# Performance work log

Hardware: AMD Instinct MI355X
Metric: run time of the kernel (lower is better)

The kernel has to match this reference:

```python
import jax, jax.numpy as jnp
import numpy as np

B, S, D, H = 4, 2048, 1024, 16
HD = D // H


def setup_inputs() -> dict:
    key = jax.random.key(0)
    ks = jax.random.split(key, 9)
    s = 0.02  # GPT-2 init scale for weights
    return {
        "hidden_states": jax.random.normal(ks[0], (B, S, D), jnp.float32),
        "Wq": jax.random.normal(ks[1], (D, D), jnp.float32) * s,
        "bq": jnp.zeros((D,), jnp.float32),
        "Wk": jax.random.normal(ks[2], (D, D), jnp.float32) * s,
        "bk": jnp.zeros((D,), jnp.float32),
        "Wv": jax.random.normal(ks[3], (D, D), jnp.float32) * s,
        "bv": jnp.zeros((D,), jnp.float32),
        "Wo": jax.random.normal(ks[4], (D, D), jnp.float32) * s,
        "bo": jnp.zeros((D,), jnp.float32),
    }


def _split_heads(x):
    b, s, _ = x.shape
    return x.reshape(b, s, H, HD).transpose(0, 2, 1, 3)  # [B,H,S,HD]


def reference(hidden_states, Wq, bq, Wk, bk, Wv, bv, Wo, bo):
    b, s, d = hidden_states.shape
    q = _split_heads(hidden_states @ Wq + bq)
    k = _split_heads(hidden_states @ Wk + bk)
    v = _split_heads(hidden_states @ Wv + bv)
    # naive attention: full [B,H,S,S] scores, scale, causal where-mask, softmax, AV
    scores = jnp.einsum('bhqd,bhkd->bhqk', q, k)
    scores = scores / jnp.asarray(HD, scores.dtype) ** 0.5  # scale_attn_weights
    causal = jnp.tril(jnp.ones((s, s), dtype=bool))  # bias buffer slice
    scores = jnp.where(causal, scores, jnp.finfo(scores.dtype).min)
    attn = jax.nn.softmax(scores, axis=-1)  # attn_dropout p=0 -> identity
    out = jnp.einsum('bhqk,bhkd->bhqd', attn, v)
    out = out.transpose(0, 2, 1, 3).reshape(b, s, d)  # merge heads
    return out @ Wo + bo  # resid_dropout p=0 -> identity
```

## Files before the change

kernel.cpp:

```cpp
#include <hip/hip_runtime.h>
#include <stdint.h>


#define GAS __attribute__((address_space(1)))
#define LAS __attribute__((address_space(3)))

typedef __attribute__((ext_vector_type(4))) float f32x4;
typedef __attribute__((ext_vector_type(8))) short bf16x8;

__device__ __forceinline__ short f2bf(float f) {
  union { float f; uint32_t u; } v; v.f = f;
  uint32_t r = v.u + 0x7fffu + ((v.u >> 16) & 1u);
  return (short)(r >> 16);
}

__device__ __forceinline__ float bf2f(short s) {
  union { uint32_t u; float f; } v;
  v.u = ((uint32_t)(uint16_t)s) << 16;
  return v.f;
}

__device__ __forceinline__ uint32_t cvt_pk_bf16(float lo, float hi) {
  uint32_t r;
  asm("v_cvt_pk_bf16_f32 %0, %1, %2" : "=v"(r) : "v"(lo), "v"(hi));
  return r;
}

__device__ __forceinline__ void gload_lds16(const void* g, void* l) {
  __builtin_amdgcn_global_load_lds((const GAS void*)g, (LAS void*)l, 16, 0, 0);
}

#define GATE(N)                                            \
  __builtin_amdgcn_sched_barrier(0);                       \
  asm volatile("s_waitcnt vmcnt(" #N ")" ::: "memory");    \
  __builtin_amdgcn_s_barrier();                            \
  __builtin_amdgcn_sched_barrier(0);

__global__ __launch_bounds__(256) void cvt_bf16_kernel(const float* __restrict__ in,
                                                       short* __restrict__ out, int n4) {
  int i = blockIdx.x * blockDim.x + threadIdx.x;
  int stride = gridDim.x * blockDim.x;
  for (int idx = i; idx < n4; idx += stride) {
    float4 v = ((const float4*)in)[idx];
    short4 o;
    o.x = f2bf(v.x); o.y = f2bf(v.y); o.z = f2bf(v.z); o.w = f2bf(v.w);
    ((short4*)out)[idx] = o;
  }
}

__global__ __launch_bounds__(256) void wt4_kernel(const float* __restrict__ W0,
                                                  const float* __restrict__ W1,
                                                  const float* __restrict__ W2,
                                                  const float* __restrict__ W3,
                                                  short* __restrict__ Wt) {
  __shared__ short tile[64][65];
  const float* W = (blockIdx.z == 0) ? W0 : (blockIdx.z == 1) ? W1
                   : (blockIdx.z == 2) ? W2 : W3;
  short* dst = Wt + ((size_t)blockIdx.z << 20);
  const int k0 = blockIdx.x * 64, n0 = blockIdx.y * 64;
  const int t = threadIdx.x;
#pragma unroll
  for (int i = 0; i < 16; ++i) {
    int r = (t >> 6) + i * 4, c = t & 63;
    tile[r][c] = f2bf(W[(size_t)(k0 + r) * 1024 + n0 + c]);
  }
  __syncthreads();
#pragma unroll
  for (int i = 0; i < 16; ++i) {
    int r = (t >> 6) + i * 4, c = t & 63;
    dst[(size_t)(n0 + r) * 1024 + k0 + c] = tile[c][r];
  }
}

template <int MODE>
__global__ __launch_bounds__(256, 3) void gemm2(const short* __restrict__ A,
                                                const short* __restrict__ Bt,
                                                const float* __restrict__ b0,
                                                const float* __restrict__ b1,
                                                const float* __restrict__ b2,
                                                void* __restrict__ O0,
                                                void* __restrict__ O1,
                                                void* __restrict__ O2) {
  __shared__ short lds[3][8192];
  const int xcd = (int)blockIdx.x & 7;
  const int t = (int)blockIdx.x >> 3;
  const int m0 = (xcd * 8 + (t & 7)) * 128;
  const int n0 = (t >> 3) * 128;
  const int tid = threadIdx.x;
  const int lane = tid & 63, w = tid >> 6;
  const int l15 = lane & 15, lg = lane >> 4;
  const int wm = w >> 1, wn = w & 1;

  const short* ag[2];
  const short* bg[2];
#pragma unroll
  for (int i = 0; i < 2; ++i) {
    const int P = w * 64 + i * 256 + lane;
    const int L = P ^ ((P >> 3) & 7);
    ag[i] = A + (size_t)(m0 + (L >> 2)) * 1024 + (L & 3) * 8;
    bg[i] = Bt + (size_t)(n0 + (L >> 2)) * 1024 + (L & 3) * 8;
  }

  int aof[4], bof[4];
#pragma unroll
  for (int mf = 0; mf < 4; ++mf) {
    const int L = (wm * 64 + mf * 16 + l15) * 4 + lg;
    aof[mf] = (L ^ ((L >> 3) & 7)) * 8;
  }
#pragma unroll
  for (int nf = 0; nf < 4; ++nf) {
    const int L = (wn * 64 + nf * 16 + l15) * 4 + lg;
    bof[nf] = (L ^ ((L >> 3) & 7)) * 8;
  }

  f32x4 acc[4][4];
#pragma unroll
  for (int i = 0; i < 4; ++i)
#pragma unroll
    for (int j = 0; j < 4; ++j) acc[i][j] = (f32x4){0.f, 0.f, 0.f, 0.f};

  auto stage = [&](int bi, int kt) {
    short* As = &lds[bi][0];
    short* Bs = &lds[bi][4096];
#pragma unroll
    for (int i = 0; i < 2; ++i) {
      gload_lds16(ag[i] + kt * 32, As + (w * 64 + i * 256) * 8);
      gload_lds16(bg[i] + kt * 32, Bs + (w * 64 + i * 256) * 8);
    }
  };

  auto compute = [&](int bi) {
    const short* As = &lds[bi][0];
    const short* Bs = &lds[bi][4096];
    bf16x8 a[4], b[4];
#pragma unroll
    for (int mf = 0; mf < 4; ++mf) a[mf] = *(const bf16x8*)&As[aof[mf]];
#pragma unroll
    for (int nf = 0; nf < 4; ++nf) b[nf] = *(const bf16x8*)&Bs[bof[nf]];
    __builtin_amdgcn_s_setprio(1);
#pragma unroll
    for (int mf = 0; mf < 4; ++mf)
#pragma unroll
      for (int nf = 0; nf < 4; ++nf)
        acc[mf][nf] =
            __builtin_amdgcn_mfma_f32_16x16x32_bf16(a[mf], b[nf], acc[mf][nf], 0, 0, 0);
    __builtin_amdgcn_s_setprio(0);
  };

  stage(0, 0);
  stage(1, 1);

  int bi = 0;
  for (int j = 0; j < 30; ++j) {
    GATE(4)
    int nb = bi + 2; if (nb >= 3) nb -= 3;
    stage(nb, j + 2);
    compute(bi);
    bi = bi + 1 == 3 ? 0 : bi + 1;
  }
  GATE(4) compute(bi);
  bi = bi + 1 == 3 ? 0 : bi + 1;
  GATE(0) compute(bi);

  if (MODE == 1) {
    float* dst = (float*)O0;
#pragma unroll
    for (int mf = 0; mf < 4; ++mf)
#pragma unroll
      for (int nf = 0; nf < 4; ++nf) {
        const int col = n0 + wn * 64 + nf * 16 + l15;
        const float bv = b0[col];
#pragma unroll
        for (int rr = 0; rr < 4; ++rr) {
          const int row = m0 + wm * 64 + mf * 16 + lg * 4 + rr;
          dst[(size_t)row * 1024 + col] = acc[mf][nf][rr] + bv;
        }
      }
  } else {
    const int mat = n0 >> 10;
    const int nc0 = n0 & 1023;
    const float* bias = (mat == 0) ? b0 : (mat == 1) ? b1 : b2;
    if (mat < 2) {
      short* dst = (short*)(mat == 0 ? O0 : O1);
#pragma unroll
      for (int mf = 0; mf < 4; ++mf)
#pragma unroll
        for (int nf = 0; nf < 4; ++nf) {
          const int col = nc0 + wn * 64 + nf * 16 + l15;
          const float bv = bias[col];
          const int h = col >> 6, hd = col & 63;
#pragma unroll
          for (int rr = 0; rr < 4; ++rr) {
            const int row = m0 + wm * 64 + mf * 16 + lg * 4 + rr;
            const int b = row >> 11, s = row & 2047;
            dst[((size_t)(b * 16 + h) * 2048 + s) * 64 + hd] = f2bf(acc[mf][nf][rr] + bv);
          }
        }
    } else {
      short* dst = (short*)O2;
#pragma unroll
      for (int mf = 0; mf < 4; ++mf) {
        const int rowb = m0 + wm * 64 + mf * 16 + lg * 4;
        const int b = rowb >> 11, s = rowb & 2047;
        const int s2 = (s & ~31) | (((s >> 2) & 3) << 3) | (((s >> 4) & 1) << 2);
#pragma unroll
        for (int nf = 0; nf < 4; ++nf) {
          const int col = nc0 + wn * 64 + nf * 16 + l15;
          const float bv = bias[col];
          const int h = col >> 6, hd = col & 63;
          short4 sv;
          sv.x = f2bf(acc[mf][nf][0] + bv);
          sv.y = f2bf(acc[mf][nf][1] + bv);
          sv.z = f2bf(acc[mf][nf][2] + bv);
          sv.w = f2bf(acc[mf][nf][3] + bv);
          *(short4*)&dst[((size_t)(b * 16 + h) * 64 + hd) * 2048 + s2] = sv;
        }
      }
    }
  }
}

__global__ __launch_bounds__(256) void attn_kernel(const short* __restrict__ Q,
                                                   const short* __restrict__ K,
                                                   const short* __restrict__ Vt,
                                                   short* __restrict__ Oout) {
  __shared__ short Ks[3][4096];
  __shared__ short Vs[3][4096];
  const int g = (int)blockIdx.x;
  const int bh = (((g >> 3) & 7) << 3) | (g & 7);
  const int jq = 15 - (g >> 6);
  const int q0 = jq * 128;
  const int tid = threadIdx.x;
  const int lane = tid & 63, w = tid >> 6;
  const int l15 = lane & 15, lg = lane >> 4;
  const short* Qb = Q + (size_t)bh * 2048 * 64;
  const short* Kb = K + (size_t)bh * 2048 * 64;
  const short* Vb = Vt + (size_t)bh * 64 * 2048;
  const int b = bh >> 4, h = bh & 15;
  const float SC = 0.18033688011112042f;
  const int qg0 = q0 + w * 32;

  bf16x8 qf[2][2];
#pragma unroll
  for (int qs = 0; qs < 2; ++qs)
#pragma unroll
    for (int kk = 0; kk < 2; ++kk) {
      bf16x8 rq =
          *(const bf16x8*)&Qb[(size_t)(qg0 + qs * 16 + l15) * 64 + kk * 32 + lg * 8];
      union { uint32_t u[4]; bf16x8 v; } sq;
#pragma unroll
      for (int d = 0; d < 4; ++d)
        sq.u[d] = cvt_pk_bf16(bf2f(rq[2 * d]) * SC, bf2f(rq[2 * d + 1]) * SC);
      qf[qs][kk] = sq.v;
    }

  union { short s[8]; bf16x8 v; } one_u;
#pragma unroll
  for (int i = 0; i < 8; ++i) one_u.s[i] = (short)0x3F80;

  const short* kg[2];
  const short* vg[2];
#pragma unroll
  for (int i = 0; i < 2; ++i) {
    const int P = (w * 2 + i) * 64 + lane;
    const int L = P ^ ((P >> 3) & 7);
    kg[i] = Kb + (size_t)(L >> 3) * 64 + (L & 7) * 8;
    vg[i] = Vb + (size_t)(L >> 3) * 2048 + (L & 7) * 8;
  }

  int kcol[2], vcol[2];
#pragma unroll
  for (int kk = 0; kk < 2; ++kk) {
    kcol[kk] = (((kk * 4 + lg) ^ (l15 & 7)) << 3);
    vcol[kk] = kcol[kk];
  }

  f32x4 o[2][4];
#pragma unroll
  for (int i = 0; i < 2; ++i)
#pragma unroll
    for (int j = 0; j < 4; ++j) o[i][j] = (f32x4){0.f, 0.f, 0.f, 0.f};
  f32x4 psacc[2] = {(f32x4){0.f, 0.f, 0.f, 0.f}, (f32x4){0.f, 0.f, 0.f, 0.f}};

  auto stageKV = [&](int bi, int kt) {
#pragma unroll
    for (int i = 0; i < 2; ++i) {
      gload_lds16(kg[i] + (size_t)kt * 4096, &Ks[bi][(w * 2 + i) * 512]);
      gload_lds16(vg[i] + kt * 64, &Vs[bi][(w * 2 + i) * 512]);
    }
  };

  const int nkt = 2 * jq + 2;
  stageKV(0, 0);
  stageKV(1, 1);

  int cur = 0;
  for (int kt = 0; kt < nkt; ++kt) {
    if (kt + 1 < nkt) {
      GATE(4)
    } else {
      GATE(0)
    }
    if (kt + 2 < nkt) {
      int nb = cur + 2; if (nb >= 3) nb -= 3;
      stageKV(nb, kt + 2);
    }

    if (kt * 64 <= qg0 + 31) {
      const short* Kc = &Ks[cur][0];
      const short* Vc = &Vs[cur][0];

      f32x4 sacc[4][2];
#pragma unroll
      for (int t = 0; t < 4; ++t)
#pragma unroll
        for (int qs = 0; qs < 2; ++qs) sacc[t][qs] = (f32x4){0.f, 0.f, 0.f, 0.f};
      __builtin_amdgcn_s_setprio(1);
#pragma unroll
      for (int t = 0; t < 4; ++t) {
        const int krow = (t * 16 + l15) * 64;
#pragma unroll
        for (int kk = 0; kk < 2; ++kk) {
          bf16x8 kf = *(const bf16x8*)&Kc[krow + kcol[kk]];
#pragma unroll
          for (int qs = 0; qs < 2; ++qs)
            sacc[t][qs] = __builtin_amdgcn_mfma_f32_16x16x32_bf16(kf, qf[qs][kk],
                                                                  sacc[t][qs], 0, 0, 0);
        }
      }
      __builtin_amdgcn_s_setprio(0);

      if (kt * 64 + 63 > qg0) {
#pragma unroll
        for (int t = 0; t < 4; ++t)
#pragma unroll
          for (int qs = 0; qs < 2; ++qs)
#pragma unroll
            for (int r = 0; r < 4; ++r) {
              const int kg_ = kt * 64 + t * 16 + lg * 4 + r;
              const int qg = qg0 + qs * 16 + l15;
              if (kg_ > qg) sacc[t][qs][r] = -3e38f;
            }
      }

      bf16x8 pa[2][2];
#pragma unroll
      for (int qs = 0; qs < 2; ++qs) {
#pragma unroll
        for (int t = 0; t < 4; ++t)
#pragma unroll
          for (int r = 0; r < 4; ++r)
            sacc[t][qs][r] = __builtin_amdgcn_exp2f(sacc[t][qs][r]);
#pragma unroll
        for (int kk = 0; kk < 2; ++kk) {
          union { uint32_t u[4]; bf16x8 v; } pw;
          pw.u[0] = cvt_pk_bf16(sacc[2 * kk][qs][0], sacc[2 * kk][qs][1]);
          pw.u[1] = cvt_pk_bf16(sacc[2 * kk][qs][2], sacc[2 * kk][qs][3]);
          pw.u[2] = cvt_pk_bf16(sacc[2 * kk + 1][qs][0], sacc[2 * kk + 1][qs][1]);
          pw.u[3] = cvt_pk_bf16(sacc[2 * kk + 1][qs][2], sacc[2 * kk + 1][qs][3]);
          pa[qs][kk] = pw.v;
        }
      }

      __builtin_amdgcn_s_setprio(1);
#pragma unroll
      for (int ds = 0; ds < 4; ++ds) {
        const int vrow = (ds * 16 + l15) * 64;
#pragma unroll
        for (int kk = 0; kk < 2; ++kk) {
          bf16x8 vf = *(const bf16x8*)&Vc[vrow + vcol[kk]];
#pragma unroll
          for (int qs = 0; qs < 2; ++qs)
            o[qs][ds] = __builtin_amdgcn_mfma_f32_16x16x32_bf16(pa[qs][kk], vf,
                                                                o[qs][ds], 0, 0, 0);
        }
      }
#pragma unroll
      for (int qs = 0; qs < 2; ++qs)
#pragma unroll
        for (int kk = 0; kk < 2; ++kk)
          psacc[qs] = __builtin_amdgcn_mfma_f32_16x16x32_bf16(pa[qs][kk], one_u.v,
                                                              psacc[qs], 0, 0, 0);
      __builtin_amdgcn_s_setprio(0);
    }

    cur = cur + 1 == 3 ? 0 : cur + 1;
  }

#pragma unroll
  for (int qs = 0; qs < 2; ++qs) {
    float inv[4];
#pragma unroll
    for (int r = 0; r < 4; ++r) inv[r] = 1.f / psacc[qs][r];
#pragma unroll
    for (int ds = 0; ds < 4; ++ds)
#pragma unroll
      for (int r = 0; r < 4; ++r) {
        const int qg = q0 + w * 32 + qs * 16 + lg * 4 + r;
        const int col = h * 64 + ds * 16 + l15;
        Oout[((size_t)(b * 2048 + qg)) * 1024 + col] = f2bf(o[qs][ds][r] * inv[r]);
      }
  }
}

extern "C" void kernel_launch(void* const* d_in, const int* in_sizes, int n_in,
                              void* d_out, int out_size, void* d_ws, size_t ws_size,
                              hipStream_t stream) {
  const float* hs = (const float*)d_in[0];
  const float* Wq = (const float*)d_in[1];
  const float* bq = (const float*)d_in[2];
  const float* Wk = (const float*)d_in[3];
  const float* bk = (const float*)d_in[4];
  const float* Wv = (const float*)d_in[5];
  const float* bv = (const float*)d_in[6];
  const float* Wo = (const float*)d_in[7];
  const float* bo = (const float*)d_in[8];

  char* ws = (char*)d_ws;
  short* Xbf = (short*)(ws + 0);
  short* Qb  = (short*)(ws + ((size_t)16 << 20));
  short* Kb  = (short*)(ws + ((size_t)32 << 20));
  short* Vtb = (short*)(ws + ((size_t)48 << 20));
  short* Wts = (short*)(ws + ((size_t)64 << 20));
  short* Wot = Wts + ((size_t)3 << 20);

  cvt_bf16_kernel<<<2048, 256, 0, stream>>>(hs, Xbf, (8192 * 1024) / 4);
  wt4_kernel<<<dim3(16, 16, 4), 256, 0, stream>>>(Wq, Wk, Wv, Wo, Wts);

  gemm2<0><<<1536, 256, 0, stream>>>(Xbf, Wts, bq, bk, bv, Qb, Kb, Vtb);

  attn_kernel<<<1024, 256, 0, stream>>>(Qb, Kb, Vtb, Xbf);

  gemm2<1><<<512, 256, 0, stream>>>(Xbf, Wot, bo, nullptr, nullptr,
                                    (float*)d_out, nullptr, nullptr);
}
```

Before: 155.9 us.

## Switch projection GEMMs to 256x128 tiles with 8 waves and phased MFMA schedule

Replaces the 128x128, 4-wave GEMM with a 256x128 tile per 512-thread block and a K-step of 64 instead of 32. It uses a new XOR-swizzled LDS layout and a four-phase loop where each wave's global-to-LDS staging is interleaved with MFMA groups, separated by barriers and priority bumps. The larger tile and deeper K step are meant to raise operand reuse and halve loop iterations, hiding load latency behind MFMA work. In exchange, LDS use triples to 144KB per block across three buffers, occupancy is lower, and the extra barriers per iteration may stall.

New measurement: 148.6 us. -4.7%, faster.

```diff
diff --git a/kernel.cpp b/kernel.cpp
--- a/kernel.cpp
+++ b/kernel.cpp
@@ -73,7 +73,7 @@
 }
 
 template <int MODE>
-__global__ __launch_bounds__(256, 3) void gemm2(const short* __restrict__ A,
+__global__ __launch_bounds__(512, 2) void gemm8(const short* __restrict__ A,
                                                 const short* __restrict__ Bt,
                                                 const float* __restrict__ b0,
                                                 const float* __restrict__ b1,
@@ -81,36 +81,38 @@
                                                 void* __restrict__ O0,
                                                 void* __restrict__ O1,
                                                 void* __restrict__ O2) {
-  __shared__ short lds[3][8192];
+  __shared__ short lds[3][24576];
   const int xcd = (int)blockIdx.x & 7;
   const int t = (int)blockIdx.x >> 3;
-  const int m0 = (xcd * 8 + (t & 7)) * 128;
-  const int n0 = (t >> 3) * 128;
+  const int m0 = (xcd * 4 + (t & 3)) * 256;
+  const int n0 = (t >> 2) * 128;
   const int tid = threadIdx.x;
   const int lane = tid & 63, w = tid >> 6;
   const int l15 = lane & 15, lg = lane >> 4;
   const int wm = w >> 1, wn = w & 1;
 
-  const short* ag[2];
+  const short* ag[4];
+#pragma unroll
+  for (int i = 0; i < 4; ++i) {
+    const int P = i * 512 + tid;
+    const int row = P >> 3, cl = (P & 7) ^ (row & 7);
+    ag[i] = A + (size_t)(m0 + row) * 1024 + cl * 8;
+  }
   const short* bg[2];
 #pragma unroll
   for (int i = 0; i < 2; ++i) {
-    const int P = w * 64 + i * 256 + lane;
-    const int L = P ^ ((P >> 3) & 7);
-    ag[i] = A + (size_t)(m0 + (L >> 2)) * 1024 + (L & 3) * 8;
-    bg[i] = Bt + (size_t)(n0 + (L >> 2)) * 1024 + (L & 3) * 8;
+    const int P = i * 512 + tid;
+    const int row = P >> 3, cl = (P & 7) ^ (row & 7);
+    bg[i] = Bt + (size_t)(n0 + row) * 1024 + cl * 8;
   }
 
   int aof[4], bof[4];
 #pragma unroll
-  for (int mf = 0; mf < 4; ++mf) {
-    const int L = (wm * 64 + mf * 16 + l15) * 4 + lg;
-    aof[mf] = (L ^ ((L >> 3) & 7)) * 8;
-  }
-#pragma unroll
-  for (int nf = 0; nf < 4; ++nf) {
-    const int L = (wn * 64 + nf * 16 + l15) * 4 + lg;
-    bof[nf] = (L ^ ((L >> 3) & 7)) * 8;
+  for (int f = 0; f < 4; ++f) {
+    const int ra = wm * 64 + f * 16 + l15;
+    aof[f] = ra * 64 + ((lg ^ (l15 & 7)) * 8);
+    const int rb = wn * 64 + f * 16 + l15;
+    bof[f] = 16384 + rb * 64 + ((lg ^ (l15 & 7)) * 8);
   }
 
   f32x4 acc[4][4];
@@ -119,48 +121,69 @@
 #pragma unroll
     for (int j = 0; j < 4; ++j) acc[i][j] = (f32x4){0.f, 0.f, 0.f, 0.f};
 
-  auto stage = [&](int bi, int kt) {
-    short* As = &lds[bi][0];
-    short* Bs = &lds[bi][4096];
-#pragma unroll
-    for (int i = 0; i < 2; ++i) {
-      gload_lds16(ag[i] + kt * 32, As + (w * 64 + i * 256) * 8);
-      gload_lds16(bg[i] + kt * 32, Bs + (w * 64 + i * 256) * 8);
-    }
+  auto stageA = [&](int bi_, int kt, int i) {
+    gload_lds16(ag[i] + kt * 64, &lds[bi_][(i * 512 + w * 64) * 8]);
   };
-
-  auto compute = [&](int bi) {
-    const short* As = &lds[bi][0];
-    const short* Bs = &lds[bi][4096];
-    bf16x8 a[4], b[4];
-#pragma unroll
-    for (int mf = 0; mf < 4; ++mf) a[mf] = *(const bf16x8*)&As[aof[mf]];
-#pragma unroll
-    for (int nf = 0; nf < 4; ++nf) b[nf] = *(const bf16x8*)&Bs[bof[nf]];
-    __builtin_amdgcn_s_setprio(1);
-#pragma unroll
-    for (int mf = 0; mf < 4; ++mf)
-#pragma unroll
-      for (int nf = 0; nf < 4; ++nf)
-        acc[mf][nf] =
-            __builtin_amdgcn_mfma_f32_16x16x32_bf16(a[mf], b[nf], acc[mf][nf], 0, 0, 0);
-    __builtin_amdgcn_s_setprio(0);
+  auto stageB = [&](int bi_, int kt, int i) {
+    gload_lds16(bg[i] + kt * 64, &lds[bi_][16384 + (i * 512 + w * 64) * 8]);
   };
-
-  stage(0, 0);
-  stage(1, 1);
-
+  auto stageTile = [&](int bi_, int kt) {
+    stageA(bi_, kt, 0); stageA(bi_, kt, 1); stageA(bi_, kt, 2); stageA(bi_, kt, 3);
+    stageB(bi_, kt, 0); stageB(bi_, kt, 1);
+  };
+
+#define RA(mf, kk) (*(const bf16x8*)&lds[bi][aof[mf] ^ ((kk) * 32)])
+#define RB(nf, kk) (*(const bf16x8*)&lds[bi][bof[nf] ^ ((kk) * 32)])
+#define MM(mf, nf)                                                             \
+  acc[mf][nf] = __builtin_amdgcn_mfma_f32_16x16x32_bf16(af[mf][0], bfr[nf][0], \
+                                                        acc[mf][nf], 0, 0, 0); \
+  acc[mf][nf] = __builtin_amdgcn_mfma_f32_16x16x32_bf16(af[mf][1], bfr[nf][1], \
+                                                        acc[mf][nf], 0, 0, 0);
+#define PH_SYNC                     \
+  __builtin_amdgcn_s_barrier();     \
+  __builtin_amdgcn_s_setprio(1);
+#define PH_END                      \
+  __builtin_amdgcn_s_setprio(0);    \
+  __builtin_amdgcn_s_barrier();
+
+  stageTile(0, 0);
+  stageTile(1, 1);
+
+  bf16x8 af[4][2], bfr[4][2];
   int bi = 0;
-  for (int j = 0; j < 30; ++j) {
-    GATE(4)
-    int nb = bi + 2; if (nb >= 3) nb -= 3;
-    stage(nb, j + 2);
-    compute(bi);
-    bi = bi + 1 == 3 ? 0 : bi + 1;
-  }
-  GATE(4) compute(bi);
-  bi = bi + 1 == 3 ? 0 : bi + 1;
-  GATE(0) compute(bi);
+  for (int j = 0; j < 16; ++j) {
+    if (j < 15) { GATE(6) } else { GATE(0) }
+    const int nb = (bi + 2 >= 3) ? bi - 1 : bi + 2;
+    const int ktn = j + 2;
+    const bool st = (j < 14);
+
+    af[0][0] = RA(0, 0); af[0][1] = RA(0, 1);
+    af[1][0] = RA(1, 0); af[1][1] = RA(1, 1);
+    bfr[0][0] = RB(0, 0); bfr[0][1] = RB(0, 1);
+    bfr[1][0] = RB(1, 0); bfr[1][1] = RB(1, 1);
+    if (st) { stageA(nb, ktn, 0); stageA(nb, ktn, 1); }
+    PH_SYNC; MM(0, 0) MM(0, 1) MM(1, 0) MM(1, 1) PH_END;
+
+    af[2][0] = RA(2, 0); af[2][1] = RA(2, 1);
+    af[3][0] = RA(3, 0); af[3][1] = RA(3, 1);
+    if (st) { stageA(nb, ktn, 2); stageA(nb, ktn, 3); }
+    PH_SYNC; MM(2, 0) MM(2, 1) MM(3, 0) MM(3, 1) PH_END;
+
+    bfr[2][0] = RB(2, 0); bfr[2][1] = RB(2, 1);
+    bfr[3][0] = RB(3, 0); bfr[3][1] = RB(3, 1);
+    if (st) stageB(nb, ktn, 0);
+    PH_SYNC; MM(2, 2) MM(2, 3) MM(3, 2) MM(3, 3) PH_END;
+
+    if (st) stageB(nb, ktn, 1);
+    PH_SYNC; MM(0, 2) MM(0, 3) MM(1, 2) MM(1, 3) PH_END;
+
+    bi = (bi + 1 == 3) ? 0 : bi + 1;
+  }
+#undef RA
+#undef RB
+#undef MM
+#undef PH_SYNC
+#undef PH_END
 
   if (MODE == 1) {
     float* dst = (float*)O0;
@@ -427,10 +450,10 @@
   cvt_bf16_kernel<<<2048, 256, 0, stream>>>(hs, Xbf, (8192 * 1024) / 4);
   wt4_kernel<<<dim3(16, 16, 4), 256, 0, stream>>>(Wq, Wk, Wv, Wo, Wts);
 
-  gemm2<0><<<1536, 256, 0, stream>>>(Xbf, Wts, bq, bk, bv, Qb, Kb, Vtb);
+  gemm8<0><<<768, 512, 0, stream>>>(Xbf, Wts, bq, bk, bv, Qb, Kb, Vtb);
 
   attn_kernel<<<1024, 256, 0, stream>>>(Qb, Kb, Vtb, Xbf);
 
-  gemm2<1><<<512, 256, 0, stream>>>(Xbf, Wot, bo, nullptr, nullptr,
+  gemm8<1><<<256, 512, 0, stream>>>(Xbf, Wot, bo, nullptr, nullptr,
                                     (float*)d_out, nullptr, nullptr);
 }
```
